# Optimization experiments

Hardware: AMD Instinct MI355X
Metric: run time of the kernel (lower is better)

## Reference

```python
import jax, jax.numpy as jnp
import numpy as np

G, N, DEG = 64, 2048, 8          # graphs, nodes/graph, avg degree
NTOT = G * N                      # 131072 nodes
E = NTOT * DEG                    # 1048576 edges
K = int(np.ceil(0.2 * N))         # 410 nodes kept per graph (SAGPooling ratio=0.2)
NK = G * K                        # 26240 pooled nodes
H, C = 3, 20                      # GAT heads, per-head channels
NEG_BIG = jnp.float32(-1e30)


def gcn(x, src, dst, W, b, n):
    """PyG GCNConv: x' = D^-1/2 (A+I) D^-1/2 x W + b (edge weight 1)."""
    h = x @ W
    deg = jax.ops.segment_sum(jnp.ones(src.shape[0], x.dtype), dst, num_segments=n) + 1.0
    dinv = jax.lax.rsqrt(deg)
    coef = dinv[src] * dinv[dst]                    # [E]
    agg = jax.ops.segment_sum(h[src] * coef[:, None], dst, num_segments=n)
    agg = agg + h * (dinv * dinv)[:, None]          # self loops
    return agg + b


def setup_inputs() -> dict:
    key = jax.random.key(0)
    ks = jax.random.split(key, 16)
    # edges constrained within each graph: per-graph local indices + offsets
    off = jnp.repeat(jnp.arange(G, dtype=jnp.int32) * N, N * DEG)   # [E]
    src = jax.random.randint(ks[0], (E,), 0, N, dtype=jnp.int32) + off
    dst = jax.random.randint(ks[1], (E,), 0, N, dtype=jnp.int32) + off
    batch = jnp.repeat(jnp.arange(G, dtype=jnp.int32), N)           # [NTOT]
    x = jax.random.normal(ks[2], (NTOT, 5), jnp.float32)
    s = 0.1
    return {
        "x": x, "src": src, "dst": dst, "batch": batch,
        "W1": jax.random.normal(ks[3], (5, 10)) * s,   "b1": jnp.zeros((10,)),
        "Ws": jax.random.normal(ks[4], (10, 1)) * s,   "bs": jnp.zeros((1,)),
        "Wg": jax.random.normal(ks[5], (10, H * C)) * s,
        "a_src": jax.random.normal(ks[6], (H, C)) * s,
        "a_dst": jax.random.normal(ks[7], (H, C)) * s,
        "bg": jnp.zeros((H * C,)),
        "Wf1": jax.random.normal(ks[8], (60, 30)) * s, "bf1": jnp.zeros((30,)),
        "Wf2": jax.random.normal(ks[9], (30, 3)) * s,  "bf2": jnp.zeros((3,)),
    }


def reference(x, src, dst, batch, W1, b1, Ws, bs, Wg, a_src, a_dst, bg, Wf1, bf1, Wf2, bf2):
    n = x.shape[0]
    # GCNConv(5,10)
    x1 = gcn(x, src, dst, W1, b1, n)                              # [NTOT,10]
    # SAGPooling: GCN scorer, top-k per graph, gate by tanh(score)
    score = gcn(x1, src, dst, Ws, bs, n)[:, 0]                    # [NTOT]
    _, topi = jax.lax.top_k(score.reshape(G, N), K)               # [G,K]
    perm = (topi + (jnp.arange(G) * N)[:, None]).reshape(-1)      # [NK] global ids
    xp = x1[perm] * jnp.tanh(score[perm])[:, None]                # [NK,10]
    # remap edges; drop (mask) edges touching removed nodes (filter_adj)
    new_idx = jnp.full((n,), -1, jnp.int32).at[perm].set(jnp.arange(NK, dtype=jnp.int32))
    s2, d2 = new_idx[src], new_idx[dst]
    emask = (s2 >= 0) & (d2 >= 0)
    s2 = jnp.where(emask, s2, 0)
    d2 = jnp.where(emask, d2, 0)
    # GATConv(10, 20, heads=3) with self loops
    h = (xp @ Wg).reshape(NK, H, C)
    al_s = jnp.sum(h * a_src, -1)                                 # [NK,H]
    al_d = jnp.sum(h * a_dst, -1)
    loop = jnp.arange(NK, dtype=jnp.int32)
    sa = jnp.concatenate([s2, loop])
    da = jnp.concatenate([d2, loop])
    ma = jnp.concatenate([emask, jnp.ones((NK,), bool)])
    logits = jax.nn.leaky_relu(al_s[sa] + al_d[da], 0.2)          # [E+NK,H]
    logits = jnp.where(ma[:, None], logits, NEG_BIG)
    mx = jax.ops.segment_max(logits, da, num_segments=NK)         # finite: self loops
    w = jnp.exp(logits - mx[da]) * ma[:, None]
    denom = jax.ops.segment_sum(w, da, num_segments=NK)
    alpha = w / denom[da]                                         # edge softmax
    out = jax.ops.segment_sum(h[sa] * alpha[..., None], da, num_segments=NK)  # [NK,H,C]
    xg = out.reshape(NK, H * C) + bg                              # concat heads -> 60
    # scatter_add readout over graphs
    g = jax.ops.segment_sum(xg, batch[perm], num_segments=G)      # [G,60]
    # MLP + LogSoftmax
    z = jax.nn.relu(g @ Wf1 + bf1) @ Wf2 + bf2                    # [G,3]
    return jax.nn.log_softmax(z, axis=1)
```

## Files before the change

### kernel.cpp

```cpp
#include <hip/hip_runtime.h>
#include <math.h>

#define G    64
#define NPG  2048
#define NTOT (G * NPG)
#define EPG  (NPG * 8)
#define NE   (NTOT * 8)
#define KSEL 410
#define NH   3
#define NC   20
#define HC   60
#define FCAP 24
#define KPAD 512
#define RP   12

#define OFF_H1P   0
#define OFF_CSR   98304
#define OFF_HIST  131072
#define OFF_RS    139264
#define OFF_SK    147456
#define OFF_NEWL  155648
#define OFF_PERML 159744
#define OFF_WSUM  160568
#define OFF_FLAGS 160632
#define ARENA_SZ  160648
#define OFF_XP    0
#define OFF_FADJ  16400
#define OFF_FCNT  36080
#define OFF_HF    37728
#define OFF_ALS   139264
#define OFF_ALD   144184
#define OFF_WRED  149104
#define OFF_GOUT  151024
#define OFF_HID   151264

__device__ inline float leaky(float x) { return x >= 0.f ? x : 0.2f * x; }

__device__ inline int wave_incl_scan(int v) {
    int lane = threadIdx.x & 63;
#pragma unroll
    for (int d = 1; d < 64; d <<= 1) {
        int t = __shfl_up(v, d, 64);
        if (lane >= d) v += t;
    }
    return v;
}

__global__ __launch_bounds__(1024) void k_all(
    const float* __restrict__ x, const int* __restrict__ src, const int* __restrict__ dst,
    const float* __restrict__ W1, const float* __restrict__ b1,
    const float* __restrict__ Ws, const float* __restrict__ bs,
    const float* __restrict__ Wg, const float* __restrict__ a_srcw,
    const float* __restrict__ a_dstw, const float* __restrict__ bg,
    const float* __restrict__ Wf1, const float* __restrict__ bf1,
    const float* __restrict__ Wf2, const float* __restrict__ bf2,
    float* __restrict__ x1g, float* __restrict__ out)
{
    __shared__ __align__(16) char arena[ARENA_SZ];
    float*          h1p   = (float*)(arena + OFF_H1P);
    unsigned short* csrL  = (unsigned short*)(arena + OFF_CSR);
    int*            hist  = (int*)(arena + OFF_HIST);
    int*            rsL   = (int*)(arena + OFF_RS);
    unsigned*       skL   = (unsigned*)(arena + OFF_SK);
    unsigned short* newLs = (unsigned short*)(arena + OFF_NEWL);
    unsigned short* permL = (unsigned short*)(arena + OFF_PERML);
    int*            wsumL = (int*)(arena + OFF_WSUM);
    int*            flags = (int*)(arena + OFF_FLAGS);
    float*          xpL   = (float*)(arena + OFF_XP);
    unsigned short* fadjL = (unsigned short*)(arena + OFF_FADJ);
    int*            fcntL = (int*)(arena + OFF_FCNT);
    float*          hfL   = (float*)(arena + OFF_HF);
    float*          alsL  = (float*)(arena + OFF_ALS);
    float*          aldL  = (float*)(arena + OFF_ALD);
    float*          wred  = (float*)(arena + OFF_WRED);
    float*          goutL = (float*)(arena + OFF_GOUT);
    float*          hidL  = (float*)(arena + OFF_HID);
#define bselS  flags[0]
#define bneedS flags[1]
#define curS   flags[2]
#define totS   flags[3]

    int g = blockIdx.x, tid = threadIdx.x, wid = tid >> 6;
    int nbase = g * NPG, ebase = g * EPG;

    for (int i = tid; i < NPG; i += 1024) hist[i] = 0;
    for (int i = tid; i < NPG; i += 1024) {
        float xi[5];
#pragma unroll
        for (int k = 0; k < 5; k++) xi[k] = x[(size_t)(nbase + i) * 5 + k];
        float v[10];
#pragma unroll
        for (int j = 0; j < 10; j++) {
            float s = 0.f;
#pragma unroll
            for (int k = 0; k < 5; k++) s += xi[k] * W1[k * 10 + j];
            v[j] = s;
        }
        float4* row = (float4*)(h1p + i * RP);
        row[0] = make_float4(v[0], v[1], v[2], v[3]);
        row[1] = make_float4(v[4], v[5], v[6], v[7]);
        row[2] = make_float4(v[8], v[9], 0.f, 0.f);
    }
    __syncthreads();
    for (int e = tid; e < EPG; e += 1024)
        atomicAdd(&hist[dst[ebase + e] - nbase], 1);
    __syncthreads();
    {
        int b2 = tid * 2;
        int v0 = hist[b2], v1 = hist[b2 + 1];
        int s = v0 + v1;
        int incl = wave_incl_scan(s);
        if ((tid & 63) == 63) wsumL[wid] = incl;
        __syncthreads();
        if (tid == 0) {
            int a = 0;
#pragma unroll
            for (int w = 0; w < 16; w++) { int t = wsumL[w]; wsumL[w] = a; a += t; }
        }
        __syncthreads();
        int base = wsumL[wid] + incl - s;
        rsL[b2] = base;
        rsL[b2 + 1] = base + v0;
        h1p[b2 * RP + 10] = rsqrtf((float)v0 + 1.0f);
        h1p[(b2 + 1) * RP + 10] = rsqrtf((float)v1 + 1.0f);
        hist[b2] = 0; hist[b2 + 1] = 0;
    }
    __syncthreads();
    for (int e = tid; e < EPG; e += 1024) {
        int ee = ebase + e;
        int sl = src[ee] - nbase;
        int dl = dst[ee] - nbase;
        int pos = rsL[dl] + atomicAdd(&hist[dl], 1);
        csrL[pos] = (unsigned short)sl;
    }
    __syncthreads();

    for (int i = tid; i < NPG; i += 1024) {
        const float4* rowi = (const float4*)(h1p + i * RP);
        float4 s0 = rowi[0], s1 = rowi[1], s2 = rowi[2];
        float di = s2.z;
        float a0 = 0.f, a1 = 0.f, a2 = 0.f, a3 = 0.f, a4 = 0.f;
        float a5 = 0.f, a6 = 0.f, a7 = 0.f, a8 = 0.f, a9 = 0.f;
        int p0 = rsL[i], p1 = (i == NPG - 1) ? EPG : rsL[i + 1];
        for (int e = p0; e < p1; e++) {
            int s = csrL[e];
            const float4* rw = (const float4*)(h1p + s * RP);
            float4 r0 = rw[0], r1 = rw[1], r2 = rw[2];
            float dv = r2.z;
            a0 += r0.x * dv; a1 += r0.y * dv; a2 += r0.z * dv; a3 += r0.w * dv;
            a4 += r1.x * dv; a5 += r1.y * dv; a6 += r1.z * dv; a7 += r1.w * dv;
            a8 += r2.x * dv; a9 += r2.y * dv;
        }
        float d2 = di * di;
        float v[10];
        v[0] = a0 * di + s0.x * d2 + b1[0];
        v[1] = a1 * di + s0.y * d2 + b1[1];
        v[2] = a2 * di + s0.z * d2 + b1[2];
        v[3] = a3 * di + s0.w * d2 + b1[3];
        v[4] = a4 * di + s1.x * d2 + b1[4];
        v[5] = a5 * di + s1.y * d2 + b1[5];
        v[6] = a6 * di + s1.z * d2 + b1[6];
        v[7] = a7 * di + s1.w * d2 + b1[7];
        v[8] = a8 * di + s2.x * d2 + b1[8];
        v[9] = a9 * di + s2.y * d2 + b1[9];
        float dot = 0.f;
#pragma unroll
        for (int j = 0; j < 10; j++) dot += v[j] * Ws[j];
        float4* xr = (float4*)(x1g + (size_t)(nbase + i) * RP);
        xr[0] = make_float4(v[0], v[1], v[2], v[3]);
        xr[1] = make_float4(v[4], v[5], v[6], v[7]);
        xr[2] = make_float4(v[8], v[9], 0.f, 0.f);
        h1p[i * RP + 11] = dot;
    }
    __syncthreads();

    float bsv = bs[0];
    for (int i = tid; i < NPG; i += 1024) {
        float2 own = *(const float2*)(h1p + i * RP + 10);
        int p0 = rsL[i], p1 = (i == NPG - 1) ? EPG : rsL[i + 1];
        float a = 0.f;
        for (int e = p0; e < p1; e++) {
            float2 dh = *(const float2*)(h1p + csrL[e] * RP + 10);
            a += dh.x * dh.y;
        }
        float sc = own.x * a + own.y * own.x * own.x + bsv;
        unsigned u = __float_as_uint(sc);
        skL[i] = (u & 0x80000000u) ? ~u : (u | 0x80000000u);
        newLs[i] = 0xFFFFu;
        hist[i] = 0;
    }
    if (tid == 0) curS = 0;
    int need = KSEL;
    unsigned prefix = 0;
    __syncthreads();

    for (int lv = 0; lv < 3; lv++) {
        for (int i = tid; i < NPG; i += 1024) {
            unsigned k = skL[i];
            bool match; unsigned bb;
            if (lv == 0)      { match = true;                  bb = k >> 21; }
            else if (lv == 1) { match = ((k >> 21) == prefix); bb = (k >> 10) & 0x7FFu; }
            else              { match = ((k >> 10) == prefix); bb = k & 0x3FFu; }
            if (match) atomicAdd(&hist[bb], 1);
        }
        __syncthreads();
        int b2 = tid * 2;
        int v0 = hist[b2], v1 = hist[b2 + 1];
        hist[b2] = 0; hist[b2 + 1] = 0;
        int s = v0 + v1;
        int incl = wave_incl_scan(s);
        if ((tid & 63) == 63) wsumL[wid] = incl;
        __syncthreads();
        if (tid == 0) {
            int a = 0;
#pragma unroll
            for (int w = 0; w < 16; w++) { int t = wsumL[w]; wsumL[w] = a; a += t; }
            totS = a;
        }
        __syncthreads();
        int base = wsumL[wid] + incl - s;
        int tot = totS;
        { int Sb = tot - base;        int Sb1 = Sb - v0; if (Sb >= need && Sb1 < need) { bselS = b2;     bneedS = need - Sb1; } }
        { int Sb = tot - (base + v0); int Sb1 = Sb - v1; if (Sb >= need && Sb1 < need) { bselS = b2 + 1; bneedS = need - Sb1; } }
        __syncthreads();
        if (lv == 0)      prefix = (unsigned)bselS;
        else if (lv == 1) prefix = (prefix << 11) | (unsigned)bselS;
        else              prefix = (prefix << 10) | (unsigned)bselS;
        need = bneedS;
        __syncthreads();
    }
    unsigned T = prefix;
    int greaterCnt = KSEL - need;

    for (int i = tid; i < NPG; i += 1024) {
        if (skL[i] > T) {
            int p = atomicAdd(&curS, 1);
            permL[p] = (unsigned short)i;
            newLs[i] = (unsigned short)p;
        }
    }
    {
        int b2 = tid * 2;
        int lc = 0, loc2[2];
#pragma unroll
        for (int k = 0; k < 2; k++)
            if (skL[b2 + k] == T) loc2[lc++] = b2 + k;
        __syncthreads();
        int incl = wave_incl_scan(lc);
        if ((tid & 63) == 63) wsumL[wid] = incl;
        __syncthreads();
        if (tid == 0) {
            int a = 0;
#pragma unroll
            for (int w = 0; w < 16; w++) { int t = wsumL[w]; wsumL[w] = a; a += t; }
        }
        __syncthreads();
        int rank0 = wsumL[wid] + incl - lc;
        for (int j = 0; j < lc; j++) {
            int rank = rank0 + j;
            if (rank < need) {
                int p = greaterCnt + rank;
                permL[p] = (unsigned short)loc2[j];
                newLs[loc2[j]] = (unsigned short)p;
            }
        }
    }
    __syncthreads();

    for (int p = tid; p < KSEL; p += 1024) {
        int iL = permL[p];
        unsigned k = skL[iL];
        unsigned u = (k & 0x80000000u) ? (k & 0x7FFFFFFFu) : ~k;
        float tt = tanhf(__uint_as_float(u));
        const float4* xr = (const float4*)(x1g + (size_t)(nbase + iL) * RP);
        float4 q0 = xr[0], q1 = xr[1], q2 = xr[2];
        float* xp = xpL + p * 10;
        xp[0] = q0.x * tt; xp[1] = q0.y * tt; xp[2] = q0.z * tt; xp[3] = q0.w * tt;
        xp[4] = q1.x * tt; xp[5] = q1.y * tt; xp[6] = q1.z * tt; xp[7] = q1.w * tt;
        xp[8] = q2.x * tt; xp[9] = q2.y * tt;
        int p0 = rsL[iL], p1 = (iL == NPG - 1) ? EPG : rsL[iL + 1];
        int c = 0;
        for (int e = p0; e < p1; e++) {
            unsigned short s2 = newLs[csrL[e]];
            if (s2 != 0xFFFFu && c < FCAP) fadjL[p * FCAP + c++] = s2;
        }
        fcntL[p] = c;
    }
    __syncthreads();

    for (int t = tid; t < KSEL * NH; t += 1024) {
        int p = t / NH, hh = t - p * NH;
        float xi[10];
#pragma unroll
        for (int k = 0; k < 10; k++) xi[k] = xpL[p * 10 + k];
        float v[NC];
        float as_ = 0.f, ad_ = 0.f;
#pragma unroll
        for (int c = 0; c < NC; c++) {
            int j = hh * NC + c;
            float vv = 0.f;
#pragma unroll
            for (int k = 0; k < 10; k++) vv += xi[k] * Wg[k * HC + j];
            v[c] = vv;
            as_ += vv * a_srcw[j];
            ad_ += vv * a_dstw[j];
        }
        float4* hr = (float4*)(hfL + p * HC + hh * NC);
#pragma unroll
        for (int q = 0; q < 5; q++)
            hr[q] = make_float4(v[4 * q], v[4 * q + 1], v[4 * q + 2], v[4 * q + 3]);
        alsL[p * NH + hh] = as_;
        aldL[p * NH + hh] = ad_;
    }
    __syncthreads();

    {
        float res[NC];
#pragma unroll
        for (int rnd = 0; rnd < 2; rnd++) {
            int task = rnd == 0 ? tid : 1024 + tid;
            bool on = rnd == 0 || tid < KPAD;
            int hh = task >> 9, p = task & (KPAD - 1);
            if (on) {
                if (p < KSEL) {
                    float aldp = aldL[p * NH + hh];
                    float lself = leaky(alsL[p * NH + hh] + aldp);
                    float m = lself;
                    int c = fcntL[p];
                    const unsigned short* f = fadjL + p * FCAP;
                    for (int e = 0; e < c; e++)
                        m = fmaxf(m, leaky(alsL[f[e] * NH + hh] + aldp));
                    float wself = expf(lself - m), wsum = wself;
                    const float4* hp = (const float4*)(hfL + p * HC + hh * NC);
                    float4 r0 = hp[0], r1 = hp[1], r2 = hp[2], r3 = hp[3], r4 = hp[4];
                    r0.x *= wself; r0.y *= wself; r0.z *= wself; r0.w *= wself;
                    r1.x *= wself; r1.y *= wself; r1.z *= wself; r1.w *= wself;
                    r2.x *= wself; r2.y *= wself; r2.z *= wself; r2.w *= wself;
                    r3.x *= wself; r3.y *= wself; r3.z *= wself; r3.w *= wself;
                    r4.x *= wself; r4.y *= wself; r4.z *= wself; r4.w *= wself;
                    for (int e = 0; e < c; e++) {
                        int s2 = f[e];
                        float w = expf(leaky(alsL[s2 * NH + hh] + aldp) - m);
                        wsum += w;
                        const float4* hq = (const float4*)(hfL + s2 * HC + hh * NC);
                        float4 t0 = hq[0], t1 = hq[1], t2 = hq[2], t3 = hq[3], t4 = hq[4];
                        r0.x += w * t0.x; r0.y += w * t0.y; r0.z += w * t0.z; r0.w += w * t0.w;
                        r1.x += w * t1.x; r1.y += w * t1.y; r1.z += w * t1.z; r1.w += w * t1.w;
                        r2.x += w * t2.x; r2.y += w * t2.y; r2.z += w * t2.z; r2.w += w * t2.w;
                        r3.x += w * t3.x; r3.y += w * t3.y; r3.z += w * t3.z; r3.w += w * t3.w;
                        r4.x += w * t4.x; r4.y += w * t4.y; r4.z += w * t4.z; r4.w += w * t4.w;
                    }
                    float inv = 1.f / wsum;
                    res[0] = r0.x * inv;  res[1] = r0.y * inv;  res[2] = r0.z * inv;  res[3] = r0.w * inv;
                    res[4] = r1.x * inv;  res[5] = r1.y * inv;  res[6] = r1.z * inv;  res[7] = r1.w * inv;
                    res[8] = r2.x * inv;  res[9] = r2.y * inv;  res[10] = r2.z * inv; res[11] = r2.w * inv;
                    res[12] = r3.x * inv; res[13] = r3.y * inv; res[14] = r3.z * inv; res[15] = r3.w * inv;
                    res[16] = r4.x * inv; res[17] = r4.y * inv; res[18] = r4.z * inv; res[19] = r4.w * inv;
                } else {
#pragma unroll
                    for (int cc = 0; cc < NC; cc++) res[cc] = 0.f;
                }
#pragma unroll
                for (int cc = 0; cc < NC; cc++) {
                    float v = res[cc];
#pragma unroll
                    for (int d = 1; d < 64; d <<= 1) v += __shfl_xor(v, d, 64);
                    res[cc] = v;
                }
                if ((tid & 63) == 0) {
                    int slot = rnd == 0 ? hh * 8 + (wid & 7) : 16 + wid;
#pragma unroll
                    for (int cc = 0; cc < NC; cc++) wred[slot * NC + cc] = res[cc];
                }
            }
        }
    }
    __syncthreads();
    if (tid < HC) {
        int hh = tid / NC, c = tid - hh * NC;
        float a = 0.f;
#pragma unroll
        for (int w = 0; w < 8; w++) a += wred[(hh * 8 + w) * NC + c];
        goutL[tid] = a + (float)KSEL * bg[tid];
    }
    __syncthreads();

    if (tid < 30) {
        float s = bf1[tid];
#pragma unroll
        for (int k = 0; k < HC; k++) s += goutL[k] * Wf1[k * 30 + tid];
        hidL[tid] = s > 0.f ? s : 0.f;
    }
    __syncthreads();
    if (tid == 0) {
        float z[3];
#pragma unroll
        for (int j = 0; j < 3; j++) {
            float s = bf2[j];
            for (int k = 0; k < 30; k++) s += hidL[k] * Wf2[k * 3 + j];
            z[j] = s;
        }
        float m = fmaxf(z[0], fmaxf(z[1], z[2]));
        float lse = logf(expf(z[0] - m) + expf(z[1] - m) + expf(z[2] - m)) + m;
#pragma unroll
        for (int j = 0; j < 3; j++) out[g * 3 + j] = z[j] - lse;
    }
}

extern "C" void kernel_launch(void* const* d_in, const int* in_sizes, int n_in,
                              void* d_out, int out_size, void* d_ws, size_t ws_size,
                              hipStream_t stream) {
    const float* x     = (const float*)d_in[0];
    const int*   src   = (const int*)d_in[1];
    const int*   dst   = (const int*)d_in[2];
    const float* W1    = (const float*)d_in[4];
    const float* b1    = (const float*)d_in[5];
    const float* Ws    = (const float*)d_in[6];
    const float* bs    = (const float*)d_in[7];
    const float* Wg    = (const float*)d_in[8];
    const float* a_src = (const float*)d_in[9];
    const float* a_dst = (const float*)d_in[10];
    const float* bg    = (const float*)d_in[11];
    const float* Wf1   = (const float*)d_in[12];
    const float* bf1   = (const float*)d_in[13];
    const float* Wf2   = (const float*)d_in[14];
    const float* bf2   = (const float*)d_in[15];
    float* out = (float*)d_out;

    float* x1g = (float*)d_ws;

    k_all<<<G, 1024, 0, stream>>>(x, src, dst, W1, b1, Ws, bs, Wg, a_src, a_dst,
                                  bg, Wf1, bf1, Wf2, bf2, x1g, out);
}
```

Baseline: 141.4 us.

## Split fused kernel into quarter-graph GCN kernel and per-graph remainder kernel

The single 64-block kernel is split in two. The first GCN layer now runs in 256 blocks, each owning a quarter of a graph's destination nodes with a local CSR, and two threads share each node's neighbour loop. The scorer GCN and the pooled adjacency build in the second kernel switch from CSR traversal to edge-parallel atomic scatters into shared memory, so no CSR is needed there. This is meant to use more of the chip for the first phase and to shrink shared memory in the second kernel. In exchange each quarter block re-reads all of its graph's edges and recomputes the degree histogram, there is an extra launch, and the float atomics make summation order nondeterministic.

```diff
diff --git a/kernel.cpp b/kernel.cpp
--- a/kernel.cpp
+++ b/kernel.cpp
@@ -14,25 +14,33 @@
 #define KPAD 512
 #define RP   12
 
-#define OFF_H1P   0
-#define OFF_CSR   98304
-#define OFF_HIST  131072
-#define OFF_RS    139264
-#define OFF_SK    147456
-#define OFF_NEWL  155648
-#define OFF_PERML 159744
-#define OFF_WSUM  160568
-#define OFF_FLAGS 160632
-#define ARENA_SZ  160648
-#define OFF_XP    0
-#define OFF_FADJ  16400
-#define OFF_FCNT  36080
-#define OFF_HF    37728
-#define OFF_ALS   139264
-#define OFF_ALD   144184
-#define OFF_WRED  149104
-#define OFF_GOUT  151024
-#define OFF_HID   151264
+#define A1_H1P   0
+#define A1_HIST  98304
+#define A1_RSQ   106496
+#define A1_CURQ  108560
+#define A1_CSRQ  110608
+#define A1_WSUM  143376
+#define A1_SZ    143440
+
+#define A2_PR    0
+#define A2_XP    0
+#define A2_DI    8192
+#define A2_SUM   16384
+#define A2_FADJ  16400
+#define A2_FCNT  36080
+#define A2_SK    37728
+#define A2_ALS   37728
+#define A2_ALD   42648
+#define A2_HIST  45920
+#define A2_WRED  47568
+#define A2_GOUT  49488
+#define A2_HID   49728
+#define A2_NEWL  54112
+#define A2_PERML 58208
+#define A2_WSUM  59032
+#define A2_FLAGS 59096
+#define A2_HF    59120
+#define A2_SZ    157520
 
 __device__ inline float leaky(float x) { return x >= 0.f ? x : 0.2f * x; }
 
@@ -46,42 +54,22 @@
     return v;
 }
 
-__global__ __launch_bounds__(1024) void k_all(
+__global__ __launch_bounds__(1024) void k1_gcn(
     const float* __restrict__ x, const int* __restrict__ src, const int* __restrict__ dst,
-    const float* __restrict__ W1, const float* __restrict__ b1,
-    const float* __restrict__ Ws, const float* __restrict__ bs,
-    const float* __restrict__ Wg, const float* __restrict__ a_srcw,
-    const float* __restrict__ a_dstw, const float* __restrict__ bg,
-    const float* __restrict__ Wf1, const float* __restrict__ bf1,
-    const float* __restrict__ Wf2, const float* __restrict__ bf2,
-    float* __restrict__ x1g, float* __restrict__ out)
+    const float* __restrict__ W1, const float* __restrict__ b1, const float* __restrict__ Ws,
+    float* __restrict__ x1g)
 {
-    __shared__ __align__(16) char arena[ARENA_SZ];
-    float*          h1p   = (float*)(arena + OFF_H1P);
-    unsigned short* csrL  = (unsigned short*)(arena + OFF_CSR);
-    int*            hist  = (int*)(arena + OFF_HIST);
-    int*            rsL   = (int*)(arena + OFF_RS);
-    unsigned*       skL   = (unsigned*)(arena + OFF_SK);
-    unsigned short* newLs = (unsigned short*)(arena + OFF_NEWL);
-    unsigned short* permL = (unsigned short*)(arena + OFF_PERML);
-    int*            wsumL = (int*)(arena + OFF_WSUM);
-    int*            flags = (int*)(arena + OFF_FLAGS);
-    float*          xpL   = (float*)(arena + OFF_XP);
-    unsigned short* fadjL = (unsigned short*)(arena + OFF_FADJ);
-    int*            fcntL = (int*)(arena + OFF_FCNT);
-    float*          hfL   = (float*)(arena + OFF_HF);
-    float*          alsL  = (float*)(arena + OFF_ALS);
-    float*          aldL  = (float*)(arena + OFF_ALD);
-    float*          wred  = (float*)(arena + OFF_WRED);
-    float*          goutL = (float*)(arena + OFF_GOUT);
-    float*          hidL  = (float*)(arena + OFF_HID);
-#define bselS  flags[0]
-#define bneedS flags[1]
-#define curS   flags[2]
-#define totS   flags[3]
-
-    int g = blockIdx.x, tid = threadIdx.x, wid = tid >> 6;
-    int nbase = g * NPG, ebase = g * EPG;
+    __shared__ __align__(16) char arena[A1_SZ];
+    float*          h1p   = (float*)(arena + A1_H1P);
+    int*            hist  = (int*)(arena + A1_HIST);
+    int*            rsQ   = (int*)(arena + A1_RSQ);
+    int*            curQ  = (int*)(arena + A1_CURQ);
+    unsigned short* csrQ  = (unsigned short*)(arena + A1_CSRQ);
+    int*            wsumL = (int*)(arena + A1_WSUM);
+
+    int bx = blockIdx.x, tid = threadIdx.x, wid = tid >> 6;
+    int g = bx & 63, q = bx >> 6;
+    int nbase = g * NPG, ebase = g * EPG, qbase = q << 9;
 
     for (int i = tid; i < NPG; i += 1024) hist[i] = 0;
     for (int i = tid; i < NPG; i += 1024) {
@@ -105,45 +93,39 @@
     for (int e = tid; e < EPG; e += 1024)
         atomicAdd(&hist[dst[ebase + e] - nbase], 1);
     __syncthreads();
-    {
-        int b2 = tid * 2;
-        int v0 = hist[b2], v1 = hist[b2 + 1];
-        int s = v0 + v1;
-        int incl = wave_incl_scan(s);
-        if ((tid & 63) == 63) wsumL[wid] = incl;
-        __syncthreads();
-        if (tid == 0) {
-            int a = 0;
-#pragma unroll
-            for (int w = 0; w < 16; w++) { int t = wsumL[w]; wsumL[w] = a; a += t; }
-        }
-        __syncthreads();
-        int base = wsumL[wid] + incl - s;
-        rsL[b2] = base;
-        rsL[b2 + 1] = base + v0;
-        h1p[b2 * RP + 10] = rsqrtf((float)v0 + 1.0f);
-        h1p[(b2 + 1) * RP + 10] = rsqrtf((float)v1 + 1.0f);
-        hist[b2] = 0; hist[b2 + 1] = 0;
-    }
+    for (int i = tid; i < NPG; i += 1024)
+        h1p[i * RP + 10] = rsqrtf((float)hist[i] + 1.0f);
+    int dvv = 0;
+    if (tid < 512) { dvv = hist[qbase + tid]; curQ[tid] = 0; }
+    int incl = wave_incl_scan(dvv);
+    if (tid < 512 && (tid & 63) == 63) wsumL[wid] = incl;
+    __syncthreads();
+    if (tid == 0) {
+        int a = 0;
+#pragma unroll
+        for (int w = 0; w < 8; w++) { int t = wsumL[w]; wsumL[w] = a; a += t; }
+        rsQ[512] = a;
+    }
+    __syncthreads();
+    if (tid < 512) rsQ[tid] = wsumL[wid] + incl - dvv;
     __syncthreads();
     for (int e = tid; e < EPG; e += 1024) {
         int ee = ebase + e;
-        int sl = src[ee] - nbase;
         int dl = dst[ee] - nbase;
-        int pos = rsL[dl] + atomicAdd(&hist[dl], 1);
-        csrL[pos] = (unsigned short)sl;
-    }
-    __syncthreads();
-
-    for (int i = tid; i < NPG; i += 1024) {
-        const float4* rowi = (const float4*)(h1p + i * RP);
-        float4 s0 = rowi[0], s1 = rowi[1], s2 = rowi[2];
-        float di = s2.z;
+        if ((dl >> 9) == q) {
+            int j = dl - qbase;
+            int pos = rsQ[j] + atomicAdd(&curQ[j], 1);
+            csrQ[pos] = (unsigned short)(src[ee] - nbase);
+        }
+    }
+    __syncthreads();
+    {
+        int p = tid >> 1, half = tid & 1, i = qbase + p;
         float a0 = 0.f, a1 = 0.f, a2 = 0.f, a3 = 0.f, a4 = 0.f;
         float a5 = 0.f, a6 = 0.f, a7 = 0.f, a8 = 0.f, a9 = 0.f;
-        int p0 = rsL[i], p1 = (i == NPG - 1) ? EPG : rsL[i + 1];
-        for (int e = p0; e < p1; e++) {
-            int s = csrL[e];
+        int p0 = rsQ[p], p1 = rsQ[p + 1];
+        for (int e = p0 + half; e < p1; e += 2) {
+            int s = csrQ[e];
             const float4* rw = (const float4*)(h1p + s * RP);
             float4 r0 = rw[0], r1 = rw[1], r2 = rw[2];
             float dv = r2.z;
@@ -151,44 +133,96 @@
             a4 += r1.x * dv; a5 += r1.y * dv; a6 += r1.z * dv; a7 += r1.w * dv;
             a8 += r2.x * dv; a9 += r2.y * dv;
         }
-        float d2 = di * di;
-        float v[10];
-        v[0] = a0 * di + s0.x * d2 + b1[0];
-        v[1] = a1 * di + s0.y * d2 + b1[1];
-        v[2] = a2 * di + s0.z * d2 + b1[2];
-        v[3] = a3 * di + s0.w * d2 + b1[3];
-        v[4] = a4 * di + s1.x * d2 + b1[4];
-        v[5] = a5 * di + s1.y * d2 + b1[5];
-        v[6] = a6 * di + s1.z * d2 + b1[6];
-        v[7] = a7 * di + s1.w * d2 + b1[7];
-        v[8] = a8 * di + s2.x * d2 + b1[8];
-        v[9] = a9 * di + s2.y * d2 + b1[9];
-        float dot = 0.f;
-#pragma unroll
-        for (int j = 0; j < 10; j++) dot += v[j] * Ws[j];
-        float4* xr = (float4*)(x1g + (size_t)(nbase + i) * RP);
-        xr[0] = make_float4(v[0], v[1], v[2], v[3]);
-        xr[1] = make_float4(v[4], v[5], v[6], v[7]);
-        xr[2] = make_float4(v[8], v[9], 0.f, 0.f);
-        h1p[i * RP + 11] = dot;
-    }
-    __syncthreads();
-
+        a0 += __shfl_xor(a0, 1, 64); a1 += __shfl_xor(a1, 1, 64);
+        a2 += __shfl_xor(a2, 1, 64); a3 += __shfl_xor(a3, 1, 64);
+        a4 += __shfl_xor(a4, 1, 64); a5 += __shfl_xor(a5, 1, 64);
+        a6 += __shfl_xor(a6, 1, 64); a7 += __shfl_xor(a7, 1, 64);
+        a8 += __shfl_xor(a8, 1, 64); a9 += __shfl_xor(a9, 1, 64);
+        if (half == 0) {
+            const float4* rowi = (const float4*)(h1p + i * RP);
+            float4 s0 = rowi[0], s1 = rowi[1], s2v = rowi[2];
+            float di = s2v.z, d2 = di * di;
+            float v[10];
+            v[0] = a0 * di + s0.x * d2 + b1[0];
+            v[1] = a1 * di + s0.y * d2 + b1[1];
+            v[2] = a2 * di + s0.z * d2 + b1[2];
+            v[3] = a3 * di + s0.w * d2 + b1[3];
+            v[4] = a4 * di + s1.x * d2 + b1[4];
+            v[5] = a5 * di + s1.y * d2 + b1[5];
+            v[6] = a6 * di + s1.z * d2 + b1[6];
+            v[7] = a7 * di + s1.w * d2 + b1[7];
+            v[8] = a8 * di + s2v.x * d2 + b1[8];
+            v[9] = a9 * di + s2v.y * d2 + b1[9];
+            float hs = 0.f;
+#pragma unroll
+            for (int j = 0; j < 10; j++) hs += v[j] * Ws[j];
+            float4* xr = (float4*)(x1g + (size_t)(nbase + i) * RP);
+            xr[0] = make_float4(v[0], v[1], v[2], v[3]);
+            xr[1] = make_float4(v[4], v[5], v[6], v[7]);
+            xr[2] = make_float4(v[8], v[9], di, hs);
+        }
+    }
+}
+
+__global__ __launch_bounds__(1024) void k2_rest(
+    const int* __restrict__ src, const int* __restrict__ dst,
+    const float* __restrict__ bs, const float* __restrict__ Wg,
+    const float* __restrict__ a_srcw, const float* __restrict__ a_dstw,
+    const float* __restrict__ bg,
+    const float* __restrict__ Wf1, const float* __restrict__ bf1,
+    const float* __restrict__ Wf2, const float* __restrict__ bf2,
+    const float* __restrict__ x1g, float* __restrict__ out)
+{
+    __shared__ __align__(16) char arena[A2_SZ];
+    float*          prL   = (float*)(arena + A2_PR);
+    float*          diL   = (float*)(arena + A2_DI);
+    float*          sumL  = (float*)(arena + A2_SUM);
+    unsigned*       skL   = (unsigned*)(arena + A2_SK);
+    int*            hist  = (int*)(arena + A2_HIST);
+    unsigned short* newLs = (unsigned short*)(arena + A2_NEWL);
+    unsigned short* permL = (unsigned short*)(arena + A2_PERML);
+    int*            wsumL = (int*)(arena + A2_WSUM);
+    int*            flags = (int*)(arena + A2_FLAGS);
+    float*          xpL   = (float*)(arena + A2_XP);
+    unsigned short* fadjL = (unsigned short*)(arena + A2_FADJ);
+    int*            fcntL = (int*)(arena + A2_FCNT);
+    float*          hfL   = (float*)(arena + A2_HF);
+    float*          alsL  = (float*)(arena + A2_ALS);
+    float*          aldL  = (float*)(arena + A2_ALD);
+    float*          wred  = (float*)(arena + A2_WRED);
+    float*          goutL = (float*)(arena + A2_GOUT);
+    float*          hidL  = (float*)(arena + A2_HID);
+#define bselS  flags[0]
+#define bneedS flags[1]
+#define curS   flags[2]
+#define totS   flags[3]
+
+    int g = blockIdx.x, tid = threadIdx.x, wid = tid >> 6;
+    int nbase = g * NPG, ebase = g * EPG;
+
+    for (int i = tid; i < NPG; i += 1024) {
+        float2 dh = *(const float2*)(x1g + (size_t)(nbase + i) * RP + 10);
+        diL[i] = dh.x;
+        prL[i] = dh.x * dh.y;
+        sumL[i] = 0.f;
+        newLs[i] = 0xFFFFu;
+        hist[i] = 0;
+    }
+    __syncthreads();
+    for (int e = tid; e < EPG; e += 1024) {
+        int ee = ebase + e;
+        int sl = src[ee] - nbase;
+        int dl = dst[ee] - nbase;
+        atomicAdd(&sumL[dl], prL[sl]);
+    }
+    __syncthreads();
     float bsv = bs[0];
     for (int i = tid; i < NPG; i += 1024) {
-        float2 own = *(const float2*)(h1p + i * RP + 10);
-        int p0 = rsL[i], p1 = (i == NPG - 1) ? EPG : rsL[i + 1];
-        float a = 0.f;
-        for (int e = p0; e < p1; e++) {
-            float2 dh = *(const float2*)(h1p + csrL[e] * RP + 10);
-            a += dh.x * dh.y;
-        }
-        float sc = own.x * a + own.y * own.x * own.x + bsv;
+        float sc = diL[i] * (sumL[i] + prL[i]) + bsv;
         unsigned u = __float_as_uint(sc);
         skL[i] = (u & 0x80000000u) ? ~u : (u | 0x80000000u);
-        newLs[i] = 0xFFFFu;
-        hist[i] = 0;
-    }
+    }
+    if (tid < KSEL) fcntL[tid] = 0;
     if (tid == 0) curS = 0;
     int need = KSEL;
     unsigned prefix = 0;
@@ -278,13 +312,15 @@
         xp[0] = q0.x * tt; xp[1] = q0.y * tt; xp[2] = q0.z * tt; xp[3] = q0.w * tt;
         xp[4] = q1.x * tt; xp[5] = q1.y * tt; xp[6] = q1.z * tt; xp[7] = q1.w * tt;
         xp[8] = q2.x * tt; xp[9] = q2.y * tt;
-        int p0 = rsL[iL], p1 = (iL == NPG - 1) ? EPG : rsL[iL + 1];
-        int c = 0;
-        for (int e = p0; e < p1; e++) {
-            unsigned short s2 = newLs[csrL[e]];
-            if (s2 != 0xFFFFu && c < FCAP) fadjL[p * FCAP + c++] = s2;
-        }
-        fcntL[p] = c;
+    }
+    for (int e = tid; e < EPG; e += 1024) {
+        int ee = ebase + e;
+        unsigned short s2 = newLs[src[ee] - nbase];
+        unsigned short d2 = newLs[dst[ee] - nbase];
+        if (s2 != 0xFFFFu && d2 != 0xFFFFu) {
+            int c = atomicAdd(&fcntL[d2], 1);
+            if (c < FCAP) fadjL[d2 * FCAP + c] = s2;
+        }
     }
     __syncthreads();
 
@@ -307,8 +343,8 @@
         }
         float4* hr = (float4*)(hfL + p * HC + hh * NC);
 #pragma unroll
-        for (int q = 0; q < 5; q++)
-            hr[q] = make_float4(v[4 * q], v[4 * q + 1], v[4 * q + 2], v[4 * q + 3]);
+        for (int qq = 0; qq < 5; qq++)
+            hr[qq] = make_float4(v[4 * qq], v[4 * qq + 1], v[4 * qq + 2], v[4 * qq + 3]);
         alsL[p * NH + hh] = as_;
         aldL[p * NH + hh] = ad_;
     }
@@ -326,7 +362,7 @@
                     float aldp = aldL[p * NH + hh];
                     float lself = leaky(alsL[p * NH + hh] + aldp);
                     float m = lself;
-                    int c = fcntL[p];
+                    int c = fcntL[p]; if (c > FCAP) c = FCAP;
                     const unsigned short* f = fadjL + p * FCAP;
                     for (int e = 0; e < c; e++)
                         m = fmaxf(m, leaky(alsL[f[e] * NH + hh] + aldp));
@@ -429,6 +465,7 @@
 
     float* x1g = (float*)d_ws;
 
-    k_all<<<G, 1024, 0, stream>>>(x, src, dst, W1, b1, Ws, bs, Wg, a_src, a_dst,
-                                  bg, Wf1, bf1, Wf2, bf2, x1g, out);
+    k1_gcn<<<G * 4, 1024, 0, stream>>>(x, src, dst, W1, b1, Ws, x1g);
+    k2_rest<<<G, 1024, 0, stream>>>(src, dst, bs, Wg, a_src, a_dst, bg,
+                                    Wf1, bf1, Wf2, bf2, x1g, out);
 }
```

Result: slower. 162.9 us (+15.2%).

## Keep GCN layer-1 output in shared memory and interleave two nodes per thread

Applied to the files above, without the earlier changes.

Layer-1 GCN outputs are written back in place into the shared h1p rows, with a barrier between gather and write, instead of going to a global workspace buffer. The later top-k gating step reads them from shared memory. This removes a global round trip and the need for d_ws. Each thread now handles its two nodes in one interleaved edge loop for ILP. The cost is extra barriers and higher register pressure.

```diff
diff --git a/kernel.cpp b/kernel.cpp
--- a/kernel.cpp
+++ b/kernel.cpp
@@ -5,7 +5,6 @@
 #define NPG  2048
 #define NTOT (G * NPG)
 #define EPG  (NPG * 8)
-#define NE   (NTOT * 8)
 #define KSEL 410
 #define NH   3
 #define NC   20
@@ -15,24 +14,24 @@
 #define RP   12
 
 #define OFF_H1P   0
+#define OFF_XP    0
+#define OFF_FADJ  16400
+#define OFF_FCNT  36080
+#define OFF_HF    37728
 #define OFF_CSR   98304
 #define OFF_HIST  131072
 #define OFF_RS    139264
+#define OFF_ALS   139264
+#define OFF_ALD   144184
 #define OFF_SK    147456
+#define OFF_WRED  149104
+#define OFF_GOUT  151024
+#define OFF_HID   151264
 #define OFF_NEWL  155648
 #define OFF_PERML 159744
 #define OFF_WSUM  160568
 #define OFF_FLAGS 160632
 #define ARENA_SZ  160648
-#define OFF_XP    0
-#define OFF_FADJ  16400
-#define OFF_FCNT  36080
-#define OFF_HF    37728
-#define OFF_ALS   139264
-#define OFF_ALD   144184
-#define OFF_WRED  149104
-#define OFF_GOUT  151024
-#define OFF_HID   151264
 
 __device__ inline float leaky(float x) { return x >= 0.f ? x : 0.2f * x; }
 
@@ -54,27 +53,27 @@
     const float* __restrict__ a_dstw, const float* __restrict__ bg,
     const float* __restrict__ Wf1, const float* __restrict__ bf1,
     const float* __restrict__ Wf2, const float* __restrict__ bf2,
-    float* __restrict__ x1g, float* __restrict__ out)
+    float* __restrict__ out)
 {
     __shared__ __align__(16) char arena[ARENA_SZ];
     float*          h1p   = (float*)(arena + OFF_H1P);
+    float*          xpL   = (float*)(arena + OFF_XP);
+    unsigned short* fadjL = (unsigned short*)(arena + OFF_FADJ);
+    int*            fcntL = (int*)(arena + OFF_FCNT);
+    float*          hfL   = (float*)(arena + OFF_HF);
     unsigned short* csrL  = (unsigned short*)(arena + OFF_CSR);
     int*            hist  = (int*)(arena + OFF_HIST);
     int*            rsL   = (int*)(arena + OFF_RS);
+    float*          alsL  = (float*)(arena + OFF_ALS);
+    float*          aldL  = (float*)(arena + OFF_ALD);
     unsigned*       skL   = (unsigned*)(arena + OFF_SK);
+    float*          wred  = (float*)(arena + OFF_WRED);
+    float*          goutL = (float*)(arena + OFF_GOUT);
+    float*          hidL  = (float*)(arena + OFF_HID);
     unsigned short* newLs = (unsigned short*)(arena + OFF_NEWL);
     unsigned short* permL = (unsigned short*)(arena + OFF_PERML);
     int*            wsumL = (int*)(arena + OFF_WSUM);
     int*            flags = (int*)(arena + OFF_FLAGS);
-    float*          xpL   = (float*)(arena + OFF_XP);
-    unsigned short* fadjL = (unsigned short*)(arena + OFF_FADJ);
-    int*            fcntL = (int*)(arena + OFF_FCNT);
-    float*          hfL   = (float*)(arena + OFF_HF);
-    float*          alsL  = (float*)(arena + OFF_ALS);
-    float*          aldL  = (float*)(arena + OFF_ALD);
-    float*          wred  = (float*)(arena + OFF_WRED);
-    float*          goutL = (float*)(arena + OFF_GOUT);
-    float*          hidL  = (float*)(arena + OFF_HID);
 #define bselS  flags[0]
 #define bneedS flags[1]
 #define curS   flags[2]
@@ -135,59 +134,98 @@
     }
     __syncthreads();
 
-    for (int i = tid; i < NPG; i += 1024) {
-        const float4* rowi = (const float4*)(h1p + i * RP);
-        float4 s0 = rowi[0], s1 = rowi[1], s2 = rowi[2];
-        float di = s2.z;
-        float a0 = 0.f, a1 = 0.f, a2 = 0.f, a3 = 0.f, a4 = 0.f;
-        float a5 = 0.f, a6 = 0.f, a7 = 0.f, a8 = 0.f, a9 = 0.f;
-        int p0 = rsL[i], p1 = (i == NPG - 1) ? EPG : rsL[i + 1];
-        for (int e = p0; e < p1; e++) {
-            int s = csrL[e];
-            const float4* rw = (const float4*)(h1p + s * RP);
-            float4 r0 = rw[0], r1 = rw[1], r2 = rw[2];
-            float dv = r2.z;
-            a0 += r0.x * dv; a1 += r0.y * dv; a2 += r0.z * dv; a3 += r0.w * dv;
-            a4 += r1.x * dv; a5 += r1.y * dv; a6 += r1.z * dv; a7 += r1.w * dv;
-            a8 += r2.x * dv; a9 += r2.y * dv;
-        }
-        float d2 = di * di;
-        float v[10];
-        v[0] = a0 * di + s0.x * d2 + b1[0];
-        v[1] = a1 * di + s0.y * d2 + b1[1];
-        v[2] = a2 * di + s0.z * d2 + b1[2];
-        v[3] = a3 * di + s0.w * d2 + b1[3];
-        v[4] = a4 * di + s1.x * d2 + b1[4];
-        v[5] = a5 * di + s1.y * d2 + b1[5];
-        v[6] = a6 * di + s1.z * d2 + b1[6];
-        v[7] = a7 * di + s1.w * d2 + b1[7];
-        v[8] = a8 * di + s2.x * d2 + b1[8];
-        v[9] = a9 * di + s2.y * d2 + b1[9];
-        float dot = 0.f;
-#pragma unroll
-        for (int j = 0; j < 10; j++) dot += v[j] * Ws[j];
-        float4* xr = (float4*)(x1g + (size_t)(nbase + i) * RP);
-        xr[0] = make_float4(v[0], v[1], v[2], v[3]);
-        xr[1] = make_float4(v[4], v[5], v[6], v[7]);
-        xr[2] = make_float4(v[8], v[9], 0.f, 0.f);
-        h1p[i * RP + 11] = dot;
-    }
-    __syncthreads();
-
-    float bsv = bs[0];
-    for (int i = tid; i < NPG; i += 1024) {
-        float2 own = *(const float2*)(h1p + i * RP + 10);
-        int p0 = rsL[i], p1 = (i == NPG - 1) ? EPG : rsL[i + 1];
-        float a = 0.f;
-        for (int e = p0; e < p1; e++) {
-            float2 dh = *(const float2*)(h1p + csrL[e] * RP + 10);
-            a += dh.x * dh.y;
-        }
-        float sc = own.x * a + own.y * own.x * own.x + bsv;
-        unsigned u = __float_as_uint(sc);
-        skL[i] = (u & 0x80000000u) ? ~u : (u | 0x80000000u);
-        newLs[i] = 0xFFFFu;
-        hist[i] = 0;
+    {
+        int i0 = tid, i1 = tid + 1024;
+        int e0 = rsL[i0], e0e = rsL[i0 + 1];
+        int e1 = rsL[i1], e1e = (i1 == NPG - 1) ? EPG : rsL[i1 + 1];
+        float acc0[10], acc1[10];
+#pragma unroll
+        for (int j = 0; j < 10; j++) { acc0[j] = 0.f; acc1[j] = 0.f; }
+        while (e0 < e0e || e1 < e1e) {
+            if (e0 < e0e) {
+                int s = csrL[e0++];
+                const float4* rw = (const float4*)(h1p + s * RP);
+                float4 r0 = rw[0], r1 = rw[1], r2 = rw[2];
+                float dv = r2.z;
+                acc0[0] += r0.x * dv; acc0[1] += r0.y * dv; acc0[2] += r0.z * dv; acc0[3] += r0.w * dv;
+                acc0[4] += r1.x * dv; acc0[5] += r1.y * dv; acc0[6] += r1.z * dv; acc0[7] += r1.w * dv;
+                acc0[8] += r2.x * dv; acc0[9] += r2.y * dv;
+            }
+            if (e1 < e1e) {
+                int s = csrL[e1++];
+                const float4* rw = (const float4*)(h1p + s * RP);
+                float4 r0 = rw[0], r1 = rw[1], r2 = rw[2];
+                float dv = r2.z;
+                acc1[0] += r0.x * dv; acc1[1] += r0.y * dv; acc1[2] += r0.z * dv; acc1[3] += r0.w * dv;
+                acc1[4] += r1.x * dv; acc1[5] += r1.y * dv; acc1[6] += r1.z * dv; acc1[7] += r1.w * dv;
+                acc1[8] += r2.x * dv; acc1[9] += r2.y * dv;
+            }
+        }
+        const float4* q0 = (const float4*)(h1p + i0 * RP);
+        const float4* q1 = (const float4*)(h1p + i1 * RP);
+        float4 s00 = q0[0], s01 = q0[1], s02 = q0[2];
+        float4 s10 = q1[0], s11 = q1[1], s12 = q1[2];
+        float di0 = s02.z, d20 = di0 * di0;
+        float di1 = s12.z, d21 = di1 * di1;
+        float b1r[10];
+#pragma unroll
+        for (int j = 0; j < 10; j++) b1r[j] = b1[j];
+        float v0[10], v1[10];
+        v0[0] = acc0[0] * di0 + s00.x * d20 + b1r[0];
+        v0[1] = acc0[1] * di0 + s00.y * d20 + b1r[1];
+        v0[2] = acc0[2] * di0 + s00.z * d20 + b1r[2];
+        v0[3] = acc0[3] * di0 + s00.w * d20 + b1r[3];
+        v0[4] = acc0[4] * di0 + s01.x * d20 + b1r[4];
+        v0[5] = acc0[5] * di0 + s01.y * d20 + b1r[5];
+        v0[6] = acc0[6] * di0 + s01.z * d20 + b1r[6];
+        v0[7] = acc0[7] * di0 + s01.w * d20 + b1r[7];
+        v0[8] = acc0[8] * di0 + s02.x * d20 + b1r[8];
+        v0[9] = acc0[9] * di0 + s02.y * d20 + b1r[9];
+        v1[0] = acc1[0] * di1 + s10.x * d21 + b1r[0];
+        v1[1] = acc1[1] * di1 + s10.y * d21 + b1r[1];
+        v1[2] = acc1[2] * di1 + s10.z * d21 + b1r[2];
+        v1[3] = acc1[3] * di1 + s10.w * d21 + b1r[3];
+        v1[4] = acc1[4] * di1 + s11.x * d21 + b1r[4];
+        v1[5] = acc1[5] * di1 + s11.y * d21 + b1r[5];
+        v1[6] = acc1[6] * di1 + s11.z * d21 + b1r[6];
+        v1[7] = acc1[7] * di1 + s11.w * d21 + b1r[7];
+        v1[8] = acc1[8] * di1 + s12.x * d21 + b1r[8];
+        v1[9] = acc1[9] * di1 + s12.y * d21 + b1r[9];
+        float hs0 = 0.f, hs1 = 0.f;
+#pragma unroll
+        for (int j = 0; j < 10; j++) { float w = Ws[j]; hs0 += v0[j] * w; hs1 += v1[j] * w; }
+        __syncthreads();
+        float4* w0 = (float4*)(h1p + i0 * RP);
+        w0[0] = make_float4(v0[0], v0[1], v0[2], v0[3]);
+        w0[1] = make_float4(v0[4], v0[5], v0[6], v0[7]);
+        w0[2] = make_float4(v0[8], v0[9], di0, hs0);
+        float4* w1 = (float4*)(h1p + i1 * RP);
+        w1[0] = make_float4(v1[0], v1[1], v1[2], v1[3]);
+        w1[1] = make_float4(v1[4], v1[5], v1[6], v1[7]);
+        w1[2] = make_float4(v1[8], v1[9], di1, hs1);
+    }
+    __syncthreads();
+
+    {
+        float bsv = bs[0];
+        int i0 = tid, i1 = tid + 1024;
+        float2 own0 = *(const float2*)(h1p + i0 * RP + 10);
+        float2 own1 = *(const float2*)(h1p + i1 * RP + 10);
+        int e0 = rsL[i0], e0e = rsL[i0 + 1];
+        int e1 = rsL[i1], e1e = (i1 == NPG - 1) ? EPG : rsL[i1 + 1];
+        float a0 = 0.f, a1 = 0.f;
+        while (e0 < e0e || e1 < e1e) {
+            if (e0 < e0e) { float2 dh = *(const float2*)(h1p + csrL[e0++] * RP + 10); a0 += dh.x * dh.y; }
+            if (e1 < e1e) { float2 dh = *(const float2*)(h1p + csrL[e1++] * RP + 10); a1 += dh.x * dh.y; }
+        }
+        float sc0 = own0.x * a0 + own0.y * own0.x * own0.x + bsv;
+        float sc1 = own1.x * a1 + own1.y * own1.x * own1.x + bsv;
+        unsigned u0 = __float_as_uint(sc0);
+        unsigned u1 = __float_as_uint(sc1);
+        skL[i0] = (u0 & 0x80000000u) ? ~u0 : (u0 | 0x80000000u);
+        skL[i1] = (u1 & 0x80000000u) ? ~u1 : (u1 | 0x80000000u);
+        newLs[i0] = 0xFFFFu; newLs[i1] = 0xFFFFu;
+        hist[i0] = 0; hist[i1] = 0;
     }
     if (tid == 0) curS = 0;
     int need = KSEL;
@@ -267,17 +305,29 @@
     }
     __syncthreads();
 
+    {
+        float4 rq0, rq1, rq2; float tt = 0.f;
+        bool havep = (tid < KSEL);
+        if (havep) {
+            int iL = permL[tid];
+            unsigned k = skL[iL];
+            unsigned u = (k & 0x80000000u) ? (k & 0x7FFFFFFFu) : ~k;
+            tt = tanhf(__uint_as_float(u));
+            const float4* xr = (const float4*)(h1p + iL * RP);
+            rq0 = xr[0]; rq1 = xr[1]; rq2 = xr[2];
+        }
+        __syncthreads();
+        if (havep) {
+            float* xp = xpL + tid * 10;
+            xp[0] = rq0.x * tt; xp[1] = rq0.y * tt; xp[2] = rq0.z * tt; xp[3] = rq0.w * tt;
+            xp[4] = rq1.x * tt; xp[5] = rq1.y * tt; xp[6] = rq1.z * tt; xp[7] = rq1.w * tt;
+            xp[8] = rq2.x * tt; xp[9] = rq2.y * tt;
+        }
+    }
+    __syncthreads();
+
     for (int p = tid; p < KSEL; p += 1024) {
         int iL = permL[p];
-        unsigned k = skL[iL];
-        unsigned u = (k & 0x80000000u) ? (k & 0x7FFFFFFFu) : ~k;
-        float tt = tanhf(__uint_as_float(u));
-        const float4* xr = (const float4*)(x1g + (size_t)(nbase + iL) * RP);
-        float4 q0 = xr[0], q1 = xr[1], q2 = xr[2];
-        float* xp = xpL + p * 10;
-        xp[0] = q0.x * tt; xp[1] = q0.y * tt; xp[2] = q0.z * tt; xp[3] = q0.w * tt;
-        xp[4] = q1.x * tt; xp[5] = q1.y * tt; xp[6] = q1.z * tt; xp[7] = q1.w * tt;
-        xp[8] = q2.x * tt; xp[9] = q2.y * tt;
         int p0 = rsL[iL], p1 = (iL == NPG - 1) ? EPG : rsL[iL + 1];
         int c = 0;
         for (int e = p0; e < p1; e++) {
@@ -426,9 +476,8 @@
     const float* Wf2   = (const float*)d_in[14];
     const float* bf2   = (const float*)d_in[15];
     float* out = (float*)d_out;
-
-    float* x1g = (float*)d_ws;
+    (void)d_ws; (void)ws_size;
 
     k_all<<<G, 1024, 0, stream>>>(x, src, dst, W1, b1, Ws, bs, Wg, a_src, a_dst,
-                                  bg, Wf1, bf1, Wf2, bf2, x1g, out);
+                                  bg, Wf1, bf1, Wf2, bf2, out);
 }
```

Result: no change. 143.7 us (+1.6%).
